# Kernel tuning notes

Hardware: AMD Instinct MI355X
Metric: run time of the kernel (lower is better)

The kernel has to match this reference:

```python
import jax, jax.numpy as jnp
import numpy as np

NUM_OBJ_CLS = 151  # Visual Genome object classes


def setup_inputs() -> dict:
    key = jax.random.key(0)
    ks = jax.random.split(key, 10)
    N_OBJ, HIDDEN, POOL, N_REL, N_RELCLS = 8192, 512, 4096, 32768, 51
    s = lambda d: 1.0 / np.sqrt(d)
    return {
        "edge_ctx": jax.random.normal(ks[0], (N_OBJ, HIDDEN), jnp.float32),
        "rel_pair_idx": jax.random.randint(ks[1], (N_REL, 2), 0, N_OBJ, jnp.int64),
        "union_features": jax.random.normal(ks[2], (N_REL, POOL), jnp.float32),
        "W_obj": jax.random.normal(ks[3], (HIDDEN, NUM_OBJ_CLS), jnp.float32) * s(HIDDEN),
        "b_obj": jnp.zeros((NUM_OBJ_CLS,), jnp.float32),
        "W_post_emb": jax.random.normal(ks[4], (HIDDEN, 2 * HIDDEN), jnp.float32) * s(HIDDEN),
        "b_post_emb": jnp.zeros((2 * HIDDEN,), jnp.float32),
        "W_post_cat": jax.random.normal(ks[5], (2 * HIDDEN, POOL), jnp.float32) * s(2 * HIDDEN),
        "b_post_cat": jnp.zeros((POOL,), jnp.float32),
        "W_rel": jax.random.normal(ks[6], (POOL, N_RELCLS), jnp.float32) * s(POOL),
        "b_rel": jnp.zeros((N_RELCLS,), jnp.float32),
        "freq_bias": jax.random.normal(ks[7], (NUM_OBJ_CLS * NUM_OBJ_CLS, N_RELCLS), jnp.float32),
    }


def reference(edge_ctx, rel_pair_idx, union_features, W_obj, b_obj,
              W_post_emb, b_post_emb, W_post_cat, b_post_cat, W_rel, b_rel,
              freq_bias):
    hidden = edge_ctx.shape[-1]
    # object classifier (stand-in for context layer's obj head)
    obj_dists = edge_ctx @ W_obj + b_obj                       # [N_obj, 151]
    obj_preds = jnp.argmax(obj_dists, axis=-1)                 # [N_obj]
    # post_emb -> split into head / tail representations
    edge_rep = (edge_ctx @ W_post_emb + b_post_emb).reshape(-1, 2, hidden)
    head_rep = edge_rep[:, 0]                                  # [N_obj, hidden]
    tail_rep = edge_rep[:, 1]
    # gather pair reps (global indices == per-image split + local gather + cat)
    h_idx, t_idx = rel_pair_idx[:, 0], rel_pair_idx[:, 1]
    prod_rep = jnp.concatenate([head_rep[h_idx], tail_rep[t_idx]], axis=-1)  # [N_rel, 2*hidden]
    prod_rep = prod_rep @ W_post_cat + b_post_cat              # [N_rel, pool]
    prod_rep = prod_rep * union_features                       # use_vision
    rel_dists = prod_rep @ W_rel + b_rel                       # [N_rel, 51]
    # frequency bias lookup on predicted (head, tail) label pairs
    pair_lbl = obj_preds[h_idx] * NUM_OBJ_CLS + obj_preds[t_idx]
    rel_dists = rel_dists + freq_bias[pair_lbl]
    return rel_dists
```

## Files before the change

kernel.cpp:

```cpp
#include <hip/hip_runtime.h>
#include <hip/hip_bf16.h>
#include <hip/hip_fp16.h>

typedef _Float16 f16;
typedef _Float16 f16x8 __attribute__((ext_vector_type(8)));
typedef _Float16 f16x4 __attribute__((ext_vector_type(4)));
typedef float f32x4 __attribute__((ext_vector_type(4)));

#define N_OBJ 8192
#define HIDDEN 512
#define POOL 4096
#define N_REL 32768
#define N_RELCLS 51
#define NUM_OBJ_CLS 151

#define WS_E16    0UL
#define WS_WPE16  8388608UL
#define WS_WCATT  9437184UL
#define WS_FT     17825792UL
#define WS_P      26214400UL
#define WS_BIAS   160432128UL
#define WS_PREDS  160448512UL
#define WS_WFRAG  160481280UL

typedef const __attribute__((address_space(1))) void* gas_ptr;
typedef __attribute__((address_space(3))) void* las_ptr;
__device__ __forceinline__ void gl_lds16(const f16* g, f16* l) {
    __builtin_amdgcn_global_load_lds((gas_ptr)g, (las_ptr)l, 16, 0, 0);
}

__global__ void k_convert(const float* __restrict__ in, f16* __restrict__ out, int n4) {
    int i = blockIdx.x * blockDim.x + threadIdx.x;
    if (i < n4) {
        f32x4 v = ((const f32x4*)in)[i];
        f16x4 h;
        h[0] = (f16)v[0]; h[1] = (f16)v[1]; h[2] = (f16)v[2]; h[3] = (f16)v[3];
        ((f16x4*)out)[i] = h;
    }
}

__global__ void k_transpose_cvt(const float* __restrict__ in, f16* __restrict__ out, int R, int C) {
    __shared__ float tile[32][33];
    int c0 = blockIdx.x * 32, r0 = blockIdx.y * 32;
    int tx = threadIdx.x, ty = threadIdx.y;
    #pragma unroll
    for (int i = 0; i < 4; i++)
        tile[ty + 8 * i][tx] = in[(size_t)(r0 + ty + 8 * i) * C + c0 + tx];
    __syncthreads();
    #pragma unroll
    for (int i = 0; i < 4; i++)
        out[(size_t)(c0 + ty + 8 * i) * R + r0 + tx] = (f16)tile[tx][ty + 8 * i];
}

__global__ __launch_bounds__(256) void k_bias(const float* __restrict__ b_pe, const float* __restrict__ Wcat,
                                              const float* __restrict__ b_cat, float* __restrict__ bias) {
    __shared__ float red[8][32];
    int c = blockIdx.x * 32 + (threadIdx.x & 31);
    int jq = threadIdx.x >> 5;
    float acc = 0.0f;
    #pragma unroll 4
    for (int j = jq * 128; j < jq * 128 + 128; j++)
        acc += b_pe[j] * Wcat[(size_t)j * POOL + c];
    red[jq][threadIdx.x & 31] = acc;
    __syncthreads();
    if (jq == 0) {
        float s = b_cat[c];
        #pragma unroll
        for (int q = 0; q < 8; q++) s += red[q][threadIdx.x & 31];
        bias[c] = s;
    }
}

#define OPB 8
__global__ __launch_bounds__(256) void k_argmax(const float* __restrict__ E, const float* __restrict__ Wobj,
                                                const float* __restrict__ bobj, int* __restrict__ preds) {
    __shared__ float se[OPB * HIDDEN];
    __shared__ double part[2][OPB][5][32];
    __shared__ double redv[OPB][32];
    __shared__ int    redj[OPB][32];
    int tid = threadIdx.x;
    int o0 = blockIdx.x * OPB;
    const f32x4* Ev = (const f32x4*)(E + (size_t)o0 * HIDDEN);
    f32x4* sev = (f32x4*)se;
    #pragma unroll
    for (int i = 0; i < OPB * HIDDEN / 4 / 256; i++)
        sev[tid + i * 256] = Ev[tid + i * 256];
    __syncthreads();

    int ks = tid >> 5;
    int jg = tid & 31;
    int jgc = (jg < 31) ? jg : 30;
    double acc[OPB][5];
    #pragma unroll
    for (int o = 0; o < OPB; o++)
        #pragma unroll
        for (int jj = 0; jj < 5; jj++) acc[o][jj] = 0.0;

    int kbase = ks * 64;
    for (int k4 = 0; k4 < 16; k4++) {
        int k = kbase + k4 * 4;
        f32x4 ev[OPB];
        #pragma unroll
        for (int o = 0; o < OPB; o++) ev[o] = *(const f32x4*)(se + o * HIDDEN + k);
        #pragma unroll
        for (int kk = 0; kk < 4; kk++) {
            const float* wrow = Wobj + (size_t)(k + kk) * NUM_OBJ_CLS;
            float wv[5];
            #pragma unroll
            for (int jj = 0; jj < 5; jj++) {
                int j = jj * 31 + jgc;
                wv[jj] = wrow[(j < NUM_OBJ_CLS) ? j : (NUM_OBJ_CLS - 1)];
            }
            #pragma unroll
            for (int o = 0; o < OPB; o++) {
                double e = (double)ev[o][kk];
                #pragma unroll
                for (int jj = 0; jj < 5; jj++)
                    acc[o][jj] = fma(e, (double)wv[jj], acc[o][jj]);
            }
        }
    }

    #pragma unroll
    for (int o = 0; o < OPB; o++)
        #pragma unroll
        for (int jj = 0; jj < 5; jj++)
            acc[o][jj] += __shfl_xor(acc[o][jj], 32);
    int w = tid >> 6, lane = tid & 63;
    if (w >= 2 && lane < 32) {
        #pragma unroll
        for (int o = 0; o < OPB; o++)
            #pragma unroll
            for (int jj = 0; jj < 5; jj++) part[w - 2][o][jj][lane] = acc[o][jj];
    }
    __syncthreads();
    if (w < 2 && lane < 32) {
        #pragma unroll
        for (int o = 0; o < OPB; o++)
            #pragma unroll
            for (int jj = 0; jj < 5; jj++) acc[o][jj] += part[w][o][jj][lane];
    }
    __syncthreads();
    if (w == 1 && lane < 32) {
        #pragma unroll
        for (int o = 0; o < OPB; o++)
            #pragma unroll
            for (int jj = 0; jj < 5; jj++) part[0][o][jj][lane] = acc[o][jj];
    }
    __syncthreads();
    if (w == 0 && lane < 31) {
        #pragma unroll
        for (int o = 0; o < OPB; o++) {
            double best = -1e300; int bj = NUM_OBJ_CLS;
            #pragma unroll
            for (int jj = 0; jj < 5; jj++) {
                int j = jj * 31 + lane;
                if (j < NUM_OBJ_CLS) {
                    double v = acc[o][jj] + part[0][o][jj][lane] + (double)bobj[j];
                    if (v > best || (v == best && j < bj)) { best = v; bj = j; }
                }
            }
            redv[o][lane] = best; redj[o][lane] = bj;
        }
    }
    __syncthreads();
    if (tid < OPB) {
        int o = tid;
        double best = -1e300; int bj = NUM_OBJ_CLS;
        for (int g = 0; g < 31; g++) {
            double v = redv[o][g]; int j = redj[o][g];
            if (v > best || (v == best && j < bj)) { best = v; bj = j; }
        }
        preds[o0 + o] = bj;
    }
}

__global__ void k_wrel_frag(const float* __restrict__ Wrel, f16* __restrict__ frag) {
    int lane = threadIdx.x & 63;
    int nt = threadIdx.x >> 6;
    int kstep = blockIdx.x;
    int n = nt * 16 + (lane & 15);
    int k0 = kstep * 32 + (lane >> 4) * 8;
    f16x8 v;
    #pragma unroll
    for (int jj = 0; jj < 8; jj++) {
        float w = (n < N_RELCLS) ? Wrel[(size_t)(k0 + jj) * N_RELCLS + n] : 0.0f;
        v[jj] = (f16)w;
    }
    ((f16x8*)frag)[(size_t)(kstep * 4 + nt) * 64 + lane] = v;
}

template<bool SPLITM>
__global__ __launch_bounds__(256) void k_gemm(const f16* __restrict__ A, const f16* __restrict__ B,
                                              f16* __restrict__ C, const float* __restrict__ bias,
                                              int K, int lda, int ldb, int ldc,
                                              long aZ, long bZ, long cZ, int biasLimit) {
    __shared__ f16 As[128 * 64];
    __shared__ f16 Bs[128 * 64];
    long z = blockIdx.z;
    A += z * aZ; B += z * bZ; C += z * cZ;

    int tid = threadIdx.x;
    int w = tid >> 6, lane = tid & 63;
    int wm = w >> 1, wn = w & 1;
    int lr = lane & 15, lg = lane >> 4;
    int mBase = blockIdx.y * 128;
    int nBase = blockIdx.x * 128;

    const f16* aSrc[4]; const f16* bSrc[4];
    f16* aDst[4]; f16* bDst[4];
    #pragma unroll
    for (int p = 0; p < 4; p++) {
        int c = p * 256 + tid;
        int row = c >> 3, slot = c & 7;
        int scol = (slot ^ (row & 7)) * 8;
        aSrc[p] = A + (size_t)(mBase + row) * lda + scol;
        bSrc[p] = B + (size_t)(nBase + row) * ldb + scol;
        aDst[p] = As + p * 2048 + w * 512;
        bDst[p] = Bs + p * 2048 + w * 512;
    }

    int swz = (lr & 7) << 4;
    f32x4 acc[4][4] = {};

    for (int k0 = 0; k0 < K; k0 += 64) {
        if (k0) __syncthreads();
        #pragma unroll
        for (int p = 0; p < 4; p++) {
            gl_lds16(aSrc[p] + k0, aDst[p]);
            gl_lds16(bSrc[p] + k0, bDst[p]);
        }
        __syncthreads();
        #pragma unroll
        for (int kh = 0; kh < 2; kh++) {
            f16x8 av[4], bv[4];
            int koff = ((kh * 64 + lg * 16) ^ swz) >> 1;
            #pragma unroll
            for (int i = 0; i < 4; i++) {
                av[i] = *(const f16x8*)(As + (wm * 64 + i * 16 + lr) * 64 + koff);
                bv[i] = *(const f16x8*)(Bs + (wn * 64 + i * 16 + lr) * 64 + koff);
            }
            #pragma unroll
            for (int i = 0; i < 4; i++)
                #pragma unroll
                for (int jj = 0; jj < 4; jj++)
                    acc[i][jj] = __builtin_amdgcn_mfma_f32_16x16x32_f16(av[i], bv[jj], acc[i][jj], 0, 0, 0);
        }
    }

    #pragma unroll
    for (int i = 0; i < 4; i++) {
        int mb = mBase + wm * 64 + i * 16 + lg * 4;
        f32x4 bi = {};
        if (bias && mb < biasLimit) bi = *(const f32x4*)(bias + mb);
        #pragma unroll
        for (int jj = 0; jj < 4; jj++) {
            int n = nBase + wn * 64 + jj * 16 + lr;
            f16x4 hv;
            #pragma unroll
            for (int r = 0; r < 4; r++) hv[r] = (f16)(acc[i][jj][r] + bi[r]);
            if (SPLITM) {
                size_t off = ((size_t)((mb >= POOL) ? N_OBJ : 0) + n) * POOL + (mb & (POOL - 1));
                *(f16x4*)(C + off) = hv;
            } else {
                *(f16x4*)(C + (size_t)n * ldc + mb) = hv;
            }
        }
    }
}

__global__ __launch_bounds__(256, 4) void k_final(const f16* __restrict__ P, const float* __restrict__ U,
                                                  const int* __restrict__ relp, const int* __restrict__ preds,
                                                  const f16* __restrict__ wfrag, const float* __restrict__ brel,
                                                  const float* __restrict__ fbias, float* __restrict__ out) {
    __shared__ f32x4 sacc[2][64][4];
    int w = threadIdx.x >> 6;
    int lane = threadIdx.x & 63;
    int rg = w & 1, kh = w >> 1;
    int lr = lane & 15, lg = lane >> 4;
    int r0 = blockIdx.x * 32 + rg * 16;
    int arow = r0 + lr;
    int h = relp[2 * arow], t = relp[2 * arow + 1];
    const f16* ph = P + (size_t)h * POOL;
    const f16* pt = P + (size_t)(N_OBJ + t) * POOL;
    const float* u = U + (size_t)arow * POOL;
    f32x4 acc[4] = {};
    int ksEnd = kh * 64 + 64;
    #pragma unroll 2
    for (int ks = kh * 64; ks < ksEnd; ks++) {
        int ka = ks * 32 + lg * 8;
        f16x8 vh = *(const f16x8*)(ph + ka);
        f16x8 vt = *(const f16x8*)(pt + ka);
        f32x4 u0 = __builtin_nontemporal_load((const f32x4*)(u + ka));
        f32x4 u1 = __builtin_nontemporal_load((const f32x4*)(u + ka + 4));
        f16x8 a;
        #pragma unroll
        for (int jj = 0; jj < 8; jj++) {
            float uu = (jj < 4) ? u0[jj] : u1[jj - 4];
            a[jj] = (f16)(((float)vh[jj] + (float)vt[jj]) * uu);
        }
        const f16x8* bf = (const f16x8*)wfrag + (size_t)ks * 4 * 64 + lane;
        #pragma unroll
        for (int nt = 0; nt < 4; nt++)
            acc[nt] = __builtin_amdgcn_mfma_f32_16x16x32_f16(a, bf[nt * 64], acc[nt], 0, 0, 0);
    }
    if (kh == 1) {
        #pragma unroll
        for (int nt = 0; nt < 4; nt++) sacc[rg][lane][nt] = acc[nt];
    }
    __syncthreads();
    if (kh == 0) {
        #pragma unroll
        for (int nt = 0; nt < 4; nt++) acc[nt] += sacc[rg][lane][nt];
        #pragma unroll
        for (int r = 0; r < 4; r++) {
            int row = r0 + lg * 4 + r;
            int h2 = relp[2 * row], t2 = relp[2 * row + 1];
            int lbl = preds[h2] * NUM_OBJ_CLS + preds[t2];
            const float* fb = fbias + (size_t)lbl * N_RELCLS;
            #pragma unroll
            for (int nt = 0; nt < 4; nt++) {
                int j = nt * 16 + lr;
                if (j < N_RELCLS)
                    out[(size_t)row * N_RELCLS + j] = acc[nt][r] + brel[j] + fb[j];
            }
        }
    }
}

extern "C" void kernel_launch(void* const* d_in, const int* in_sizes, int n_in,
                              void* d_out, int out_size, void* d_ws, size_t ws_size,
                              hipStream_t stream) {
    const float* edge_ctx = (const float*)d_in[0];
    const int*   relp     = (const int*)d_in[1];
    const float* U        = (const float*)d_in[2];
    const float* Wobj     = (const float*)d_in[3];
    const float* bobj     = (const float*)d_in[4];
    const float* Wpe      = (const float*)d_in[5];
    const float* bpe      = (const float*)d_in[6];
    const float* Wcat     = (const float*)d_in[7];
    const float* bcat     = (const float*)d_in[8];
    const float* Wrel     = (const float*)d_in[9];
    const float* brel     = (const float*)d_in[10];
    const float* fbias    = (const float*)d_in[11];
    float* out = (float*)d_out;

    char* ws = (char*)d_ws;
    f16*   E16    = (f16*)(ws + WS_E16);
    f16*   Wpe16  = (f16*)(ws + WS_WPE16);
    f16*   WcatT  = (f16*)(ws + WS_WCATT);
    f16*   FT     = (f16*)(ws + WS_FT);
    f16*   P      = (f16*)(ws + WS_P);
    float* bias   = (float*)(ws + WS_BIAS);
    int*   preds  = (int*)(ws + WS_PREDS);
    f16*   wfrag  = (f16*)(ws + WS_WFRAG);

    k_convert<<<4096, 256, 0, stream>>>(edge_ctx, E16, N_OBJ * HIDDEN / 4);
    k_convert<<<512, 256, 0, stream>>>(Wpe, Wpe16, HIDDEN * 2 * HIDDEN / 4);
    k_transpose_cvt<<<dim3(POOL / 32, (2 * HIDDEN) / 32), dim3(32, 8), 0, stream>>>(Wcat, WcatT, 2 * HIDDEN, POOL);
    k_bias<<<POOL / 32, 256, 0, stream>>>(bpe, Wcat, bcat, bias);
    k_argmax<<<N_OBJ / OPB, 256, 0, stream>>>(edge_ctx, Wobj, bobj, preds);
    k_wrel_frag<<<POOL / 32, 256, 0, stream>>>(Wrel, wfrag);
    k_gemm<false><<<dim3(POOL / 128, HIDDEN / 128, 2), 256, 0, stream>>>(
        Wpe16, WcatT, FT, nullptr, HIDDEN, 2 * HIDDEN, 2 * HIDDEN, HIDDEN,
        512L, 512L, (long)POOL * HIDDEN, 0);
    k_gemm<true><<<dim3(N_OBJ / 128, (2 * POOL) / 128, 1), 256, 0, stream>>>(
        FT, E16, P, bias, HIDDEN, HIDDEN, HIDDEN, POOL,
        0L, 0L, 0L, POOL);
    k_final<<<N_REL / 32, 256, 0, stream>>>(P, U, relp, preds, wfrag, brel, fbias, out);
}
```

Baseline: 418.9 us.

## Merge prep kernels, double-buffer GEMM LDS tiles, drop split-K in final kernel

Five small preprocessing kernels (converts, transpose, bias fold, Wrel fragment packing) are merged into one launch that dispatches on block ID, to cut launch overhead. The GEMM now uses 32-wide K tiles in two LDS buffers, issuing the next tile's global-to-LDS loads before computing on the current one, with a new XOR swizzle. The final kernel drops its two-wave split-K and LDS reduction, so each wave handles 16 rows over the full K with 64 rows per block. This gives fewer syncs per block but a longer serial K loop in each wave.

```diff
diff --git a/kernel.cpp b/kernel.cpp
--- a/kernel.cpp
+++ b/kernel.cpp
@@ -29,45 +29,74 @@
     __builtin_amdgcn_global_load_lds((gas_ptr)g, (las_ptr)l, 16, 0, 0);
 }
 
-__global__ void k_convert(const float* __restrict__ in, f16* __restrict__ out, int n4) {
-    int i = blockIdx.x * blockDim.x + threadIdx.x;
-    if (i < n4) {
-        f32x4 v = ((const f32x4*)in)[i];
-        f16x4 h;
-        h[0] = (f16)v[0]; h[1] = (f16)v[1]; h[2] = (f16)v[2]; h[3] = (f16)v[3];
-        ((f16x4*)out)[i] = h;
-    }
-}
-
-__global__ void k_transpose_cvt(const float* __restrict__ in, f16* __restrict__ out, int R, int C) {
+__global__ __launch_bounds__(256) void k_prep(const float* __restrict__ edge_ctx, const float* __restrict__ Wpe,
+                                              const float* __restrict__ Wcat, const float* __restrict__ bpe,
+                                              const float* __restrict__ bcat, const float* __restrict__ Wrel,
+                                              f16* __restrict__ E16, f16* __restrict__ Wpe16,
+                                              f16* __restrict__ WcatT, float* __restrict__ bias,
+                                              f16* __restrict__ wfrag) {
     __shared__ float tile[32][33];
-    int c0 = blockIdx.x * 32, r0 = blockIdx.y * 32;
-    int tx = threadIdx.x, ty = threadIdx.y;
-    #pragma unroll
-    for (int i = 0; i < 4; i++)
-        tile[ty + 8 * i][tx] = in[(size_t)(r0 + ty + 8 * i) * C + c0 + tx];
-    __syncthreads();
-    #pragma unroll
-    for (int i = 0; i < 4; i++)
-        out[(size_t)(c0 + ty + 8 * i) * R + r0 + tx] = (f16)tile[tx][ty + 8 * i];
-}
-
-__global__ __launch_bounds__(256) void k_bias(const float* __restrict__ b_pe, const float* __restrict__ Wcat,
-                                              const float* __restrict__ b_cat, float* __restrict__ bias) {
     __shared__ float red[8][32];
-    int c = blockIdx.x * 32 + (threadIdx.x & 31);
-    int jq = threadIdx.x >> 5;
-    float acc = 0.0f;
-    #pragma unroll 4
-    for (int j = jq * 128; j < jq * 128 + 128; j++)
-        acc += b_pe[j] * Wcat[(size_t)j * POOL + c];
-    red[jq][threadIdx.x & 31] = acc;
-    __syncthreads();
-    if (jq == 0) {
-        float s = b_cat[c];
-        #pragma unroll
-        for (int q = 0; q < 8; q++) s += red[q][threadIdx.x & 31];
-        bias[c] = s;
+    int bid = blockIdx.x, tid = threadIdx.x;
+    if (bid < 1024) {
+        const f32x4* in = (const f32x4*)edge_ctx;
+        f16x4* out = (f16x4*)E16;
+        int base = bid * 1024 + tid;
+        #pragma unroll
+        for (int s = 0; s < 4; s++) {
+            f32x4 v = in[base + s * 256];
+            f16x4 h; h[0]=(f16)v[0]; h[1]=(f16)v[1]; h[2]=(f16)v[2]; h[3]=(f16)v[3];
+            out[base + s * 256] = h;
+        }
+    } else if (bid < 1152) {
+        const f32x4* in = (const f32x4*)Wpe;
+        f16x4* out = (f16x4*)Wpe16;
+        int base = (bid - 1024) * 1024 + tid;
+        #pragma unroll
+        for (int s = 0; s < 4; s++) {
+            f32x4 v = in[base + s * 256];
+            f16x4 h; h[0]=(f16)v[0]; h[1]=(f16)v[1]; h[2]=(f16)v[2]; h[3]=(f16)v[3];
+            out[base + s * 256] = h;
+        }
+    } else if (bid < 5248) {
+        int t = bid - 1152;
+        int c0 = (t & 127) * 32, r0 = (t >> 7) * 32;
+        int tx = tid & 31, ty = tid >> 5;
+        #pragma unroll
+        for (int i = 0; i < 4; i++)
+            tile[ty + 8 * i][tx] = Wcat[(size_t)(r0 + ty + 8 * i) * POOL + c0 + tx];
+        __syncthreads();
+        #pragma unroll
+        for (int i = 0; i < 4; i++)
+            WcatT[(size_t)(c0 + ty + 8 * i) * (2 * HIDDEN) + r0 + tx] = (f16)tile[tx][ty + 8 * i];
+    } else if (bid < 5376) {
+        int c = (bid - 5248) * 32 + (tid & 31);
+        int jq = tid >> 5;
+        float acc = 0.0f;
+        #pragma unroll 4
+        for (int j = jq * 128; j < jq * 128 + 128; j++)
+            acc += bpe[j] * Wcat[(size_t)j * POOL + c];
+        red[jq][tid & 31] = acc;
+        __syncthreads();
+        if (jq == 0) {
+            float s = bcat[c];
+            #pragma unroll
+            for (int q = 0; q < 8; q++) s += red[q][tid & 31];
+            bias[c] = s;
+        }
+    } else {
+        int kstep = bid - 5376;
+        int lane = tid & 63;
+        int nt = tid >> 6;
+        int n = nt * 16 + (lane & 15);
+        int k0 = kstep * 32 + (lane >> 4) * 8;
+        f16x8 v;
+        #pragma unroll
+        for (int jj = 0; jj < 8; jj++) {
+            float w = (n < N_RELCLS) ? Wrel[(size_t)(k0 + jj) * N_RELCLS + n] : 0.0f;
+            v[jj] = (f16)w;
+        }
+        ((f16x8*)wfrag)[(size_t)(kstep * 4 + nt) * 64 + lane] = v;
     }
 }
 
@@ -175,28 +204,13 @@
     }
 }
 
-__global__ void k_wrel_frag(const float* __restrict__ Wrel, f16* __restrict__ frag) {
-    int lane = threadIdx.x & 63;
-    int nt = threadIdx.x >> 6;
-    int kstep = blockIdx.x;
-    int n = nt * 16 + (lane & 15);
-    int k0 = kstep * 32 + (lane >> 4) * 8;
-    f16x8 v;
-    #pragma unroll
-    for (int jj = 0; jj < 8; jj++) {
-        float w = (n < N_RELCLS) ? Wrel[(size_t)(k0 + jj) * N_RELCLS + n] : 0.0f;
-        v[jj] = (f16)w;
-    }
-    ((f16x8*)frag)[(size_t)(kstep * 4 + nt) * 64 + lane] = v;
-}
-
 template<bool SPLITM>
 __global__ __launch_bounds__(256) void k_gemm(const f16* __restrict__ A, const f16* __restrict__ B,
                                               f16* __restrict__ C, const float* __restrict__ bias,
                                               int K, int lda, int ldb, int ldc,
                                               long aZ, long bZ, long cZ, int biasLimit) {
-    __shared__ f16 As[128 * 64];
-    __shared__ f16 Bs[128 * 64];
+    __shared__ f16 As[2][128 * 32];
+    __shared__ f16 Bs[2][128 * 32];
     long z = blockIdx.z;
     A += z * aZ; B += z * bZ; C += z * cZ;
 
@@ -207,45 +221,50 @@
     int mBase = blockIdx.y * 128;
     int nBase = blockIdx.x * 128;
 
-    const f16* aSrc[4]; const f16* bSrc[4];
-    f16* aDst[4]; f16* bDst[4];
-    #pragma unroll
-    for (int p = 0; p < 4; p++) {
+    const f16* aSrc[2]; const f16* bSrc[2];
+    f16* aDst[2]; f16* bDst[2];
+    #pragma unroll
+    for (int p = 0; p < 2; p++) {
         int c = p * 256 + tid;
-        int row = c >> 3, slot = c & 7;
-        int scol = (slot ^ (row & 7)) * 8;
-        aSrc[p] = A + (size_t)(mBase + row) * lda + scol;
-        bSrc[p] = B + (size_t)(nBase + row) * ldb + scol;
-        aDst[p] = As + p * 2048 + w * 512;
-        bDst[p] = Bs + p * 2048 + w * 512;
-    }
-
-    int swz = (lr & 7) << 4;
+        int row = c >> 2, slot = c & 3;
+        int g = (slot ^ ((row ^ (row >> 2)) & 3)) * 8;
+        aSrc[p] = A + (size_t)(mBase + row) * lda + g;
+        bSrc[p] = B + (size_t)(nBase + row) * ldb + g;
+        aDst[p] = As[0] + p * 2048 + w * 512;
+        bDst[p] = Bs[0] + p * 2048 + w * 512;
+    }
+    int swzL = ((lr & 3) ^ ((lr >> 2) & 3)) * 8;
     f32x4 acc[4][4] = {};
-
-    for (int k0 = 0; k0 < K; k0 += 64) {
-        if (k0) __syncthreads();
-        #pragma unroll
-        for (int p = 0; p < 4; p++) {
-            gl_lds16(aSrc[p] + k0, aDst[p]);
-            gl_lds16(bSrc[p] + k0, bDst[p]);
-        }
+    int nt = K >> 5;
+
+    #pragma unroll
+    for (int p = 0; p < 2; p++) { gl_lds16(aSrc[p], aDst[p]); gl_lds16(bSrc[p], bDst[p]); }
+
+    for (int t = 0; t < nt; t++) {
         __syncthreads();
-        #pragma unroll
-        for (int kh = 0; kh < 2; kh++) {
-            f16x8 av[4], bv[4];
-            int koff = ((kh * 64 + lg * 16) ^ swz) >> 1;
-            #pragma unroll
-            for (int i = 0; i < 4; i++) {
-                av[i] = *(const f16x8*)(As + (wm * 64 + i * 16 + lr) * 64 + koff);
-                bv[i] = *(const f16x8*)(Bs + (wn * 64 + i * 16 + lr) * 64 + koff);
-            }
-            #pragma unroll
-            for (int i = 0; i < 4; i++)
-                #pragma unroll
-                for (int jj = 0; jj < 4; jj++)
-                    acc[i][jj] = __builtin_amdgcn_mfma_f32_16x16x32_f16(av[i], bv[jj], acc[i][jj], 0, 0, 0);
-        }
+        int cur = t & 1;
+        if (t + 1 < nt) {
+            int koff = (t + 1) * 32;
+            int nxt = (cur ^ 1) * 4096;
+            #pragma unroll
+            for (int p = 0; p < 2; p++) {
+                gl_lds16(aSrc[p] + koff, aDst[p] + nxt);
+                gl_lds16(bSrc[p] + koff, bDst[p] + nxt);
+            }
+        }
+        const f16* Ab = As[cur];
+        const f16* Bb = Bs[cur];
+        f16x8 av[4], bv[4];
+        #pragma unroll
+        for (int i = 0; i < 4; i++) {
+            av[i] = *(const f16x8*)(Ab + (wm * 64 + i * 16 + lr) * 32 + ((lg * 8) ^ swzL));
+            bv[i] = *(const f16x8*)(Bb + (wn * 64 + i * 16 + lr) * 32 + ((lg * 8) ^ swzL));
+        }
+        #pragma unroll
+        for (int i = 0; i < 4; i++)
+            #pragma unroll
+            for (int jj = 0; jj < 4; jj++)
+                acc[i][jj] = __builtin_amdgcn_mfma_f32_16x16x32_f16(av[i], bv[jj], acc[i][jj], 0, 0, 0);
     }
 
     #pragma unroll
@@ -269,25 +288,21 @@
     }
 }
 
-__global__ __launch_bounds__(256, 4) void k_final(const f16* __restrict__ P, const float* __restrict__ U,
-                                                  const int* __restrict__ relp, const int* __restrict__ preds,
-                                                  const f16* __restrict__ wfrag, const float* __restrict__ brel,
-                                                  const float* __restrict__ fbias, float* __restrict__ out) {
-    __shared__ f32x4 sacc[2][64][4];
+__global__ __launch_bounds__(256) void k_final(const f16* __restrict__ P, const float* __restrict__ U,
+                                               const int* __restrict__ relp, const int* __restrict__ preds,
+                                               const f16* __restrict__ wfrag, const float* __restrict__ brel,
+                                               const float* __restrict__ fbias, float* __restrict__ out) {
     int w = threadIdx.x >> 6;
     int lane = threadIdx.x & 63;
-    int rg = w & 1, kh = w >> 1;
     int lr = lane & 15, lg = lane >> 4;
-    int r0 = blockIdx.x * 32 + rg * 16;
+    int r0 = blockIdx.x * 64 + w * 16;
     int arow = r0 + lr;
     int h = relp[2 * arow], t = relp[2 * arow + 1];
     const f16* ph = P + (size_t)h * POOL;
     const f16* pt = P + (size_t)(N_OBJ + t) * POOL;
     const float* u = U + (size_t)arow * POOL;
     f32x4 acc[4] = {};
-    int ksEnd = kh * 64 + 64;
-    #pragma unroll 2
-    for (int ks = kh * 64; ks < ksEnd; ks++) {
+    for (int ks = 0; ks < POOL / 32; ks++) {
         int ka = ks * 32 + lg * 8;
         f16x8 vh = *(const f16x8*)(ph + ka);
         f16x8 vt = *(const f16x8*)(pt + ka);
@@ -304,26 +319,17 @@
         for (int nt = 0; nt < 4; nt++)
             acc[nt] = __builtin_amdgcn_mfma_f32_16x16x32_f16(a, bf[nt * 64], acc[nt], 0, 0, 0);
     }
-    if (kh == 1) {
-        #pragma unroll
-        for (int nt = 0; nt < 4; nt++) sacc[rg][lane][nt] = acc[nt];
-    }
-    __syncthreads();
-    if (kh == 0) {
-        #pragma unroll
-        for (int nt = 0; nt < 4; nt++) acc[nt] += sacc[rg][lane][nt];
-        #pragma unroll
-        for (int r = 0; r < 4; r++) {
-            int row = r0 + lg * 4 + r;
-            int h2 = relp[2 * row], t2 = relp[2 * row + 1];
-            int lbl = preds[h2] * NUM_OBJ_CLS + preds[t2];
-            const float* fb = fbias + (size_t)lbl * N_RELCLS;
-            #pragma unroll
-            for (int nt = 0; nt < 4; nt++) {
-                int j = nt * 16 + lr;
-                if (j < N_RELCLS)
-                    out[(size_t)row * N_RELCLS + j] = acc[nt][r] + brel[j] + fb[j];
-            }
+    #pragma unroll
+    for (int r = 0; r < 4; r++) {
+        int row = r0 + lg * 4 + r;
+        int h2 = relp[2 * row], t2 = relp[2 * row + 1];
+        int lbl = preds[h2] * NUM_OBJ_CLS + preds[t2];
+        const float* fb = fbias + (size_t)lbl * N_RELCLS;
+        #pragma unroll
+        for (int nt = 0; nt < 4; nt++) {
+            int j = nt * 16 + lr;
+            if (j < N_RELCLS)
+                out[(size_t)row * N_RELCLS + j] = acc[nt][r] + brel[j] + fb[j];
         }
     }
 }
@@ -355,17 +361,14 @@
     int*   preds  = (int*)(ws + WS_PREDS);
     f16*   wfrag  = (f16*)(ws + WS_WFRAG);
 
-    k_convert<<<4096, 256, 0, stream>>>(edge_ctx, E16, N_OBJ * HIDDEN / 4);
-    k_convert<<<512, 256, 0, stream>>>(Wpe, Wpe16, HIDDEN * 2 * HIDDEN / 4);
-    k_transpose_cvt<<<dim3(POOL / 32, (2 * HIDDEN) / 32), dim3(32, 8), 0, stream>>>(Wcat, WcatT, 2 * HIDDEN, POOL);
-    k_bias<<<POOL / 32, 256, 0, stream>>>(bpe, Wcat, bcat, bias);
+    k_prep<<<5504, 256, 0, stream>>>(edge_ctx, Wpe, Wcat, bpe, bcat, Wrel,
+                                     E16, Wpe16, WcatT, bias, wfrag);
     k_argmax<<<N_OBJ / OPB, 256, 0, stream>>>(edge_ctx, Wobj, bobj, preds);
-    k_wrel_frag<<<POOL / 32, 256, 0, stream>>>(Wrel, wfrag);
     k_gemm<false><<<dim3(POOL / 128, HIDDEN / 128, 2), 256, 0, stream>>>(
         Wpe16, WcatT, FT, nullptr, HIDDEN, 2 * HIDDEN, 2 * HIDDEN, HIDDEN,
         512L, 512L, (long)POOL * HIDDEN, 0);
     k_gemm<true><<<dim3(N_OBJ / 128, (2 * POOL) / 128, 1), 256, 0, stream>>>(
         FT, E16, P, bias, HIDDEN, HIDDEN, HIDDEN, POOL,
         0L, 0L, 0L, POOL);
-    k_final<<<N_REL / 32, 256, 0, stream>>>(P, U, relp, preds, wfrag, brel, fbias, out);
-}
+    k_final<<<N_REL / 64, 256, 0, stream>>>(P, U, relp, preds, wfrag, brel, fbias, out);
+}
```

After: 387.0 us. -7.6%, faster.
